# Optimization experiments

Hardware: AMD Instinct MI355X
Metric: run time of the kernel (lower is better)

## Reference

```python
import jax, jax.numpy as jnp
import numpy as np
from jax import lax

B, C_IN, C_OUT, L, K, PAD = 4, 16, 16, 1024, 5, 2


def setup_inputs() -> dict:
    key = jax.random.key(0)
    k1, k2 = jax.random.split(key)
    scores = jax.random.normal(k1, (B, C_IN, L, L), dtype=jnp.float32)
    # kaiming_uniform_(a=sqrt(5)) -> bound = 1/sqrt(fan_in), fan_in = (C_IN/groups)*K*K
    fan_in = C_IN * K * K
    bound = 1.0 / np.sqrt(fan_in)
    weight = jax.random.uniform(k2, (C_OUT, C_IN, K, K), dtype=jnp.float32,
                                minval=-bound, maxval=bound)
    bias = jnp.zeros((C_OUT,), dtype=jnp.float32)
    return {"scores": scores, "weight": weight, "bias": bias}


def reference(scores, weight, bias):
    # scores: [B, C_in, L, L]
    Lq = scores.shape[-2]
    causal = jnp.tril(jnp.ones((Lq, Lq), dtype=bool))  # [L, L]
    # mask_{-inf} then softmax over key dim
    masked = jnp.where(causal, scores, -jnp.inf)
    probs = jax.nn.softmax(masked, axis=-1)
    # grouped conv2d over the [L, L] score map (shape-preserving padding)
    out = lax.conv_general_dilated(
        probs, weight,
        window_strides=(1, 1),
        padding=((PAD, PAD), (PAD, PAD)),
        rhs_dilation=(1, 1),
        dimension_numbers=("NCHW", "OIHW", "NCHW"),
        feature_group_count=1,
    )
    out = out + bias[None, :, None, None]
    # mask_{0}: zero out non-causal positions
    out = jnp.where(causal, out, jnp.zeros((), dtype=out.dtype))
    return out
```

## Files before the change

kernel.cpp:

```cpp
#include <hip/hip_runtime.h>
#include <hip/hip_bf16.h>
#include <math.h>

#define LSEQ  1024
#define CIN   16
#define COUT  16
#define BATCH 4
#define TILE  16
#define NT    13
#define CSTR  48
#define RSTR  (20 * CSTR)

#define WFRAG_BYTES (NT * 64 * 8 * 2)
#define PROBS_ELEMS ((size_t)BATCH * CIN * LSEQ * LSEQ)
#define WS_NEEDED   (WFRAG_BYTES + PROBS_ELEMS * 2)

typedef __attribute__((ext_vector_type(8))) short short8;
typedef __attribute__((ext_vector_type(4))) float f32x4;
typedef __attribute__((ext_vector_type(4))) int   i32x4;

static __device__ __forceinline__ unsigned f2bf_u(float f) {
    unsigned u = __builtin_bit_cast(unsigned, f);
    return (u + 0x7fff + ((u >> 16) & 1)) >> 16;
}
static __device__ __forceinline__ unsigned short f2bf(float f) { return (unsigned short)f2bf_u(f); }

__global__ __launch_bounds__(256) void softmax_probs_kernel(
    const float* __restrict__ scores,
    const float* __restrict__ weight,
    ushort* __restrict__ wfrag,
    ushort* __restrict__ probs)
{
    const int tid = threadIdx.x;

    if (blockIdx.x == BATCH * LSEQ) {
        for (int slot = tid; slot < NT * 64; slot += 256) {
            const int t = slot >> 6, lane = slot & 63;
            const int co = lane & 15, q = lane >> 4;
            const int ci0 = (q & 1) * 8, cb = q >> 1;
            const int c = 2 * t + cb;
            ushort* dst = wfrag + (size_t)slot * 8;
            #pragma unroll
            for (int jj = 0; jj < 8; ++jj) {
                float wv = (c < 25) ? weight[co * (CIN * 25) + (ci0 + jj) * 25 + c] : 0.f;
                dst[jj] = f2bf(wv);
            }
        }
        return;
    }

    __shared__ ushort sm[CIN * LSEQ];

    const int bi   = blockIdx.x;
    const int b    = bi >> 10;
    const int row  = bi & (LSEQ - 1);
    const int wv   = tid >> 6;
    const int lane = tid & 63;

    #pragma unroll
    for (int m = 0; m < 4; ++m) {
        const int ci = wv * 4 + m;
        const float* rowp = scores + ((size_t)(b * CIN + ci) * LSEQ + row) * LSEQ;

        float e[16];
        #pragma unroll
        for (int c = 0; c < 4; ++c) {
            const int j0 = c * 256 + lane * 4;
            float4 v = make_float4(0.f, 0.f, 0.f, 0.f);
            if (c * 256 <= row) v = *(const float4*)(rowp + j0);
            e[c*4+0] = (j0 + 0 <= row) ? __expf(v.x) : 0.f;
            e[c*4+1] = (j0 + 1 <= row) ? __expf(v.y) : 0.f;
            e[c*4+2] = (j0 + 2 <= row) ? __expf(v.z) : 0.f;
            e[c*4+3] = (j0 + 3 <= row) ? __expf(v.w) : 0.f;
        }
        float s = 0.f;
        #pragma unroll
        for (int t = 0; t < 16; ++t) s += e[t];
        #pragma unroll
        for (int off = 32; off > 0; off >>= 1) s += __shfl_xor(s, off, 64);
        const float rinv = 1.0f / s;

        ushort* smrow = sm + ci * LSEQ;
        #pragma unroll
        for (int c = 0; c < 4; ++c) {
            if (c * 256 <= row) {
                const int j0 = c * 256 + lane * 4;
                uint2 pk;
                pk.x = f2bf_u(e[c*4+0] * rinv) | (f2bf_u(e[c*4+1] * rinv) << 16);
                pk.y = f2bf_u(e[c*4+2] * rinv) | (f2bf_u(e[c*4+3] * rinv) << 16);
                *(uint2*)(smrow + j0) = pk;
            }
        }
    }
    __syncthreads();

    ushort* prow = probs + ((size_t)b * LSEQ + row) * (LSEQ * CIN);
    const int nch = 2 * (row + 1);
    for (int chunk = tid; chunk < nch; chunk += 256) {
        const int col = chunk >> 1;
        const int h   = chunk & 1;
        i32x4 pk;
        #pragma unroll
        for (int k = 0; k < 4; ++k) {
            unsigned lo = sm[(h * 8 + 2 * k    ) * LSEQ + col];
            unsigned hi = sm[(h * 8 + 2 * k + 1) * LSEQ + col];
            pk[k] = (int)(lo | (hi << 16));
        }
        *(i32x4*)(prow + (size_t)col * CIN + h * 8) = pk;
    }
}

__global__ __launch_bounds__(256) void conv_mfma2_kernel(
    const ushort* __restrict__ probs,
    const float* __restrict__ bias,
    const ushort* __restrict__ wfrag,
    float* __restrict__ out)
{
    const int jt = blockIdx.x, it = blockIdx.y, b = blockIdx.z;
    const int j0 = jt * TILE, i0 = it * TILE;
    const int tid = threadIdx.x;

    if (jt > it) {
        #pragma unroll
        for (int vv = 0; vv < 4; ++vv) {
            int e  = vv * 256 + tid;
            int co = e >> 6, il = (e >> 2) & 15, jq = e & 3;
            *(float4*)(out + ((size_t)(b * COUT + co) * LSEQ + i0 + il) * LSEQ + j0 + jq * 4)
                = make_float4(0.f, 0.f, 0.f, 0.f);
        }
        return;
    }

    const int lane = tid & 63;
    const int w    = tid >> 6;
    const int n    = lane & 15;
    const int q    = lane >> 4;

    short8 af[NT];
    #pragma unroll
    for (int t = 0; t < NT; ++t)
        af[t] = *(const short8*)(wfrag + (size_t)(t * 64 + lane) * 8);

    float bs[4];
    #pragma unroll
    for (int r = 0; r < 4; ++r) bs[r] = bias[q * 4 + r];

    int addr[NT];
    {
        const int cb  = q >> 1;
        const int cio = (q & 1) * 16;
        #pragma unroll
        for (int t = 0; t < NT; ++t) {
            int c = 2 * t + cb;
            if (c >= 25) addr[t] = 0;
            else {
                int kh = c / 5, kw = c - kh * 5;
                addr[t] = (kh * 20 + (n + kw)) * CSTR + cio + w * (4 * RSTR);
            }
        }
    }

    __shared__ ushort ptile[20 * 20 * 24];

    const ushort* pb = probs + (size_t)b * (LSEQ * LSEQ * CIN);
    #pragma unroll
    for (int u = 0; u < 4; ++u) {
        const int e = u * 256 + tid;
        if (e < 800) {
            const int half = e & 1, cell = e >> 1;
            const int rr = cell / 20, cc = cell - rr * 20;
            const int row = i0 - 2 + rr;
            const int col = j0 - 2 + cc;
            const bool ok = (row >= 0) && (row < LSEQ) && (col >= 0) && (col < LSEQ) && (col <= row);
            i32x4 pk = {0, 0, 0, 0};
            if (ok)
                pk = *(const i32x4*)(pb + ((size_t)row * LSEQ + col) * CIN + half * 8);
            *(i32x4*)((char*)ptile + cell * CSTR + half * 16) = pk;
        }
    }
    __syncthreads();

    #pragma unroll
    for (int s = 0; s < 4; ++s) {
        f32x4 acc = {0.f, 0.f, 0.f, 0.f};
        #pragma unroll
        for (int t = 0; t < NT; ++t) {
            short8 bf = *(const short8*)((const char*)ptile + addr[t] + s * RSTR);
            acc = __builtin_amdgcn_mfma_f32_16x16x32_bf16(af[t], bf, acc, 0, 0, 0);
        }
        const int i = i0 + w * 4 + s;
        const int j = j0 + n;
        #pragma unroll
        for (int r = 0; r < 4; ++r) {
            const int co = q * 4 + r;
            out[((size_t)(b * COUT + co) * LSEQ + i) * LSEQ + j] = (j <= i) ? (acc[r] + bs[r]) : 0.f;
        }
    }
}

__global__ __launch_bounds__(256) void stats_fb_kernel(const float* __restrict__ scores,
                                                       float* __restrict__ rowinv)
{
    const int w   = blockIdx.x;
    const int row = w & (LSEQ - 1);
    const int tid = threadIdx.x;
    const int j0  = tid * 4;
    float4 v = make_float4(0.f, 0.f, 0.f, 0.f);
    if (j0 <= row) v = *(const float4*)(scores + (size_t)w * LSEQ + j0);
    float s = 0.f;
    s += (j0 + 0 <= row) ? __expf(v.x) : 0.f;
    s += (j0 + 1 <= row) ? __expf(v.y) : 0.f;
    s += (j0 + 2 <= row) ? __expf(v.z) : 0.f;
    s += (j0 + 3 <= row) ? __expf(v.w) : 0.f;
    #pragma unroll
    for (int off = 32; off > 0; off >>= 1) s += __shfl_xor(s, off, 64);
    __shared__ float part[4];
    if ((tid & 63) == 0) part[tid >> 6] = s;
    __syncthreads();
    if (tid == 0) rowinv[w] = 1.0f / (part[0] + part[1] + part[2] + part[3]);
}

__global__ void wprep_fb_kernel(const float* __restrict__ weight, ushort* __restrict__ wfrag)
{
    const int lane = threadIdx.x;
    const int co   = lane & 15;
    const int q    = lane >> 4;
    const int ci0  = (q & 1) * 8;
    const int cb   = q >> 1;
    for (int t = 0; t < NT; ++t) {
        const int c = 2 * t + cb;
        ushort* dst = wfrag + (size_t)(t * 64 + lane) * 8;
        #pragma unroll
        for (int jj = 0; jj < 8; ++jj) {
            float wv = (c < 25) ? weight[co * (CIN * 25) + (ci0 + jj) * 25 + c] : 0.f;
            dst[jj] = f2bf(wv);
        }
    }
}

__global__ __launch_bounds__(256) void conv_fb_kernel(
    const float* __restrict__ scores,
    const float* __restrict__ bias,
    const float* __restrict__ rowinv,
    const ushort* __restrict__ wfrag,
    float* __restrict__ out)
{
    const int jt = blockIdx.x, it = blockIdx.y, b = blockIdx.z;
    const int j0 = jt * TILE, i0 = it * TILE;
    const int tid = threadIdx.x;

    if (jt > it) {
        #pragma unroll
        for (int vv = 0; vv < 4; ++vv) {
            int e  = vv * 256 + tid;
            int co = e >> 6, il = (e >> 2) & 15, jq = e & 3;
            *(float4*)(out + ((size_t)(b * COUT + co) * LSEQ + i0 + il) * LSEQ + j0 + jq * 4)
                = make_float4(0.f, 0.f, 0.f, 0.f);
        }
        return;
    }

    const int lane = tid & 63;
    const int w    = tid >> 6;
    const int n    = lane & 15;
    const int q    = lane >> 4;

    short8 af[NT];
    #pragma unroll
    for (int t = 0; t < NT; ++t)
        af[t] = *(const short8*)(wfrag + (size_t)(t * 64 + lane) * 8);

    float bs[4];
    #pragma unroll
    for (int r = 0; r < 4; ++r) bs[r] = bias[q * 4 + r];

    int addr[NT];
    {
        const int cb  = q >> 1;
        const int cio = (q & 1) * 16;
        #pragma unroll
        for (int t = 0; t < NT; ++t) {
            int c = 2 * t + cb;
            if (c >= 25) addr[t] = 0;
            else {
                int kh = c / 5, kw = c - kh * 5;
                addr[t] = (kh * 20 + (n + kw)) * CSTR + cio + w * (4 * RSTR);
            }
        }
    }

    __shared__ ushort ptile[20 * 20 * 24];

    for (int u = 0; u < 8; ++u) {
        int e = u * 256 + tid;
        if (e < 1920) {
            int ci  = e / 120;
            int rem = e - ci * 120;
            int rr  = rem / 6;
            int cq  = rem - rr * 6;
            int row  = i0 - 2 + rr;
            int gcol = j0 - 4 + cq * 4;
            bool rok = (row >= 0) && (row < LSEQ);
            float rinv = 0.f;
            float4 v = make_float4(0.f, 0.f, 0.f, 0.f);
            if (rok) {
                int rid = (b * CIN + ci) * LSEQ + row;
                rinv = rowinv[rid];
                if (gcol >= 0 && gcol <= LSEQ - 4 && gcol <= row)
                    v = *(const float4*)(scores + (size_t)rid * LSEQ + gcol);
            }
            float pv[4] = {v.x, v.y, v.z, v.w};
            #pragma unroll
            for (int l = 0; l < 4; ++l) {
                int col = gcol + l;
                int cc  = cq * 4 - 2 + l;
                bool ok = rok && col >= 0 && col < LSEQ && col <= row;
                float p = ok ? __expf(pv[l]) * rinv : 0.f;
                if (cc >= 0 && cc < 20)
                    ptile[(rr * 20 + cc) * 24 + ci] = f2bf(p);
            }
        }
    }
    __syncthreads();

    #pragma unroll
    for (int s = 0; s < 4; ++s) {
        f32x4 acc = {0.f, 0.f, 0.f, 0.f};
        #pragma unroll
        for (int t = 0; t < NT; ++t) {
            short8 bf = *(const short8*)((const char*)ptile + addr[t] + s * RSTR);
            acc = __builtin_amdgcn_mfma_f32_16x16x32_bf16(af[t], bf, acc, 0, 0, 0);
        }
        const int i = i0 + w * 4 + s;
        const int j = j0 + n;
        #pragma unroll
        for (int r = 0; r < 4; ++r) {
            const int co = q * 4 + r;
            out[((size_t)(b * COUT + co) * LSEQ + i) * LSEQ + j] = (j <= i) ? (acc[r] + bs[r]) : 0.f;
        }
    }
}

extern "C" void kernel_launch(void* const* d_in, const int* in_sizes, int n_in,
                              void* d_out, int out_size, void* d_ws, size_t ws_size,
                              hipStream_t stream) {
    const float* scores = (const float*)d_in[0];
    const float* weight = (const float*)d_in[1];
    const float* bias   = (const float*)d_in[2];
    float* out = (float*)d_out;

    if (ws_size >= WS_NEEDED) {
        ushort* wfrag = (ushort*)d_ws;
        ushort* probs = (ushort*)((char*)d_ws + WFRAG_BYTES);

        softmax_probs_kernel<<<BATCH * LSEQ + 1, 256, 0, stream>>>(
            scores, weight, wfrag, probs);

        dim3 g(LSEQ / TILE, LSEQ / TILE, BATCH);
        conv_mfma2_kernel<<<g, 256, 0, stream>>>(probs, bias, wfrag, out);
    } else {
        float*  rowinv = (float*)d_ws;
        ushort* wfrag  = (ushort*)((char*)d_ws + (size_t)BATCH * CIN * LSEQ * 4);

        stats_fb_kernel<<<BATCH * CIN * LSEQ, 256, 0, stream>>>(scores, rowinv);
        wprep_fb_kernel<<<1, 64, 0, stream>>>(weight, wfrag);

        dim3 g(LSEQ / TILE, LSEQ / TILE, BATCH);
        conv_fb_kernel<<<g, 256, 0, stream>>>(scores, bias, rowinv, wfrag, out);
    }
}
```

Measured before the change: 521.2 us.

## Widen conv tile to 32 columns and swap MFMA operands for float4 stores

The conv kernel tile grows from 16x16 to 16 rows by 32 columns, so each block stages a 20x36 halo in LDS and reuses the loaded weight fragments across two 16-column subtiles. The MFMA operand order is swapped so each lane's accumulator holds four consecutive output columns for one channel, which allows vectorized float4 stores instead of scalar ones. This aims to reduce halo overhead, block count and store instructions, at the cost of more LDS per block and a coarser causal-skip granularity.

Result: no change. 530.6 us (+1.8%).

```diff
diff --git a/kernel.cpp b/kernel.cpp
--- a/kernel.cpp
+++ b/kernel.cpp
@@ -5,11 +5,14 @@
 #define LSEQ  1024
 #define CIN   16
 #define COUT  16
+#define TILE  16
+#define TJ    32
 #define BATCH 4
-#define TILE  16
 #define NT    13
 #define CSTR  48
+#define CW    36
 #define RSTR  (20 * CSTR)
+#define RSTR2 (CW * CSTR)
 
 #define WFRAG_BYTES (NT * 64 * 8 * 2)
 #define PROBS_ELEMS ((size_t)BATCH * CIN * LSEQ * LSEQ)
@@ -117,14 +120,14 @@
     float* __restrict__ out)
 {
     const int jt = blockIdx.x, it = blockIdx.y, b = blockIdx.z;
-    const int j0 = jt * TILE, i0 = it * TILE;
+    const int j0 = jt * TJ, i0 = it * TILE;
     const int tid = threadIdx.x;
 
-    if (jt > it) {
-        #pragma unroll
-        for (int vv = 0; vv < 4; ++vv) {
+    if (2 * jt > it) {
+        #pragma unroll
+        for (int vv = 0; vv < 8; ++vv) {
             int e  = vv * 256 + tid;
-            int co = e >> 6, il = (e >> 2) & 15, jq = e & 3;
+            int co = e >> 7, il = (e >> 3) & 15, jq = e & 7;
             *(float4*)(out + ((size_t)(b * COUT + co) * LSEQ + i0 + il) * LSEQ + j0 + jq * 4)
                 = make_float4(0.f, 0.f, 0.f, 0.f);
         }
@@ -141,9 +144,7 @@
     for (int t = 0; t < NT; ++t)
         af[t] = *(const short8*)(wfrag + (size_t)(t * 64 + lane) * 8);
 
-    float bs[4];
-    #pragma unroll
-    for (int r = 0; r < 4; ++r) bs[r] = bias[q * 4 + r];
+    const float bsn = bias[n];
 
     int addr[NT];
     {
@@ -155,20 +156,20 @@
             if (c >= 25) addr[t] = 0;
             else {
                 int kh = c / 5, kw = c - kh * 5;
-                addr[t] = (kh * 20 + (n + kw)) * CSTR + cio + w * (4 * RSTR);
-            }
-        }
-    }
-
-    __shared__ ushort ptile[20 * 20 * 24];
+                addr[t] = (kh * CW + (n + kw)) * CSTR + cio + w * (4 * RSTR2);
+            }
+        }
+    }
+
+    __shared__ ushort ptile[20 * CW * 24];
 
     const ushort* pb = probs + (size_t)b * (LSEQ * LSEQ * CIN);
     #pragma unroll
-    for (int u = 0; u < 4; ++u) {
+    for (int u = 0; u < 6; ++u) {
         const int e = u * 256 + tid;
-        if (e < 800) {
+        if (e < 1440) {
             const int half = e & 1, cell = e >> 1;
-            const int rr = cell / 20, cc = cell - rr * 20;
+            const int rr = cell / CW, cc = cell - rr * CW;
             const int row = i0 - 2 + rr;
             const int col = j0 - 2 + cc;
             const bool ok = (row >= 0) && (row < LSEQ) && (col >= 0) && (col < LSEQ) && (col <= row);
@@ -182,18 +183,22 @@
 
     #pragma unroll
     for (int s = 0; s < 4; ++s) {
-        f32x4 acc = {0.f, 0.f, 0.f, 0.f};
-        #pragma unroll
-        for (int t = 0; t < NT; ++t) {
-            short8 bf = *(const short8*)((const char*)ptile + addr[t] + s * RSTR);
-            acc = __builtin_amdgcn_mfma_f32_16x16x32_bf16(af[t], bf, acc, 0, 0, 0);
-        }
         const int i = i0 + w * 4 + s;
-        const int j = j0 + n;
-        #pragma unroll
-        for (int r = 0; r < 4; ++r) {
-            const int co = q * 4 + r;
-            out[((size_t)(b * COUT + co) * LSEQ + i) * LSEQ + j] = (j <= i) ? (acc[r] + bs[r]) : 0.f;
+        #pragma unroll
+        for (int sub = 0; sub < 2; ++sub) {
+            f32x4 acc = {0.f, 0.f, 0.f, 0.f};
+            #pragma unroll
+            for (int t = 0; t < NT; ++t) {
+                short8 pf = *(const short8*)((const char*)ptile + addr[t] + s * RSTR2 + sub * (16 * CSTR));
+                acc = __builtin_amdgcn_mfma_f32_16x16x32_bf16(pf, af[t], acc, 0, 0, 0);
+            }
+            const int jb = j0 + sub * 16 + q * 4;
+            float4 v;
+            v.x = (jb + 0 <= i) ? acc[0] + bsn : 0.f;
+            v.y = (jb + 1 <= i) ? acc[1] + bsn : 0.f;
+            v.z = (jb + 2 <= i) ? acc[2] + bsn : 0.f;
+            v.w = (jb + 3 <= i) ? acc[3] + bsn : 0.f;
+            *(float4*)(out + ((size_t)(b * COUT + n) * LSEQ + i) * LSEQ + jb) = v;
         }
     }
 }
@@ -356,7 +361,7 @@
         softmax_probs_kernel<<<BATCH * LSEQ + 1, 256, 0, stream>>>(
             scores, weight, wfrag, probs);
 
-        dim3 g(LSEQ / TILE, LSEQ / TILE, BATCH);
+        dim3 g(LSEQ / TJ, LSEQ / TILE, BATCH);
         conv_mfma2_kernel<<<g, 256, 0, stream>>>(probs, bias, wfrag, out);
     } else {
         float*  rowinv = (float*)d_ws;
```

## Load conv probability tile via global_load_lds and swap MFMA operands for vector stores

Applied to the files above, without the earlier changes.

The conv kernel now stages the 20x20 probability halo tile straight from global memory into LDS with global_load_lds, using a dense 32-byte cell stride. Out-of-range cells read from a zeroed pad placed after the weight fragments instead of being masked in registers. The MFMA operands are swapped so each lane holds four consecutive output columns for one channel, which lets the epilogue write float4 stores instead of scalar strided ones. The risks are that the removed LDS padding may bring back bank conflicts, and that the LDS destination layout must match what global_load_lds actually writes per wave.

After: 536.9 us. +3.0%, slower.

```diff
diff --git a/kernel.cpp b/kernel.cpp
--- a/kernel.cpp
+++ b/kernel.cpp
@@ -5,15 +5,18 @@
 #define LSEQ  1024
 #define CIN   16
 #define COUT  16
+#define TILE  16
 #define BATCH 4
-#define TILE  16
 #define NT    13
+#define CSTR2 32
+#define RSTR2 (20 * CSTR2)
 #define CSTR  48
 #define RSTR  (20 * CSTR)
 
 #define WFRAG_BYTES (NT * 64 * 8 * 2)
+#define ZPAD_BYTES  64
 #define PROBS_ELEMS ((size_t)BATCH * CIN * LSEQ * LSEQ)
-#define WS_NEEDED   (WFRAG_BYTES + PROBS_ELEMS * 2)
+#define WS_NEEDED   (WFRAG_BYTES + ZPAD_BYTES + PROBS_ELEMS * 2)
 
 typedef __attribute__((ext_vector_type(8))) short short8;
 typedef __attribute__((ext_vector_type(4))) float f32x4;
@@ -46,6 +49,7 @@
                 dst[jj] = f2bf(wv);
             }
         }
+        if (tid < 32) wfrag[NT * 64 * 8 + tid] = 0;
         return;
     }
 
@@ -141,9 +145,7 @@
     for (int t = 0; t < NT; ++t)
         af[t] = *(const short8*)(wfrag + (size_t)(t * 64 + lane) * 8);
 
-    float bs[4];
-    #pragma unroll
-    for (int r = 0; r < 4; ++r) bs[r] = bias[q * 4 + r];
+    const float bsn = bias[n];
 
     int addr[NT];
     {
@@ -155,28 +157,33 @@
             if (c >= 25) addr[t] = 0;
             else {
                 int kh = c / 5, kw = c - kh * 5;
-                addr[t] = (kh * 20 + (n + kw)) * CSTR + cio + w * (4 * RSTR);
-            }
-        }
-    }
-
-    __shared__ ushort ptile[20 * 20 * 24];
+                addr[t] = ((w * 4 + kh) * 20 + (n + kw)) * CSTR2 + cio;
+            }
+        }
+    }
+
+    __shared__ ushort ptile[1024 * 8];
 
     const ushort* pb = probs + (size_t)b * (LSEQ * LSEQ * CIN);
+    const ushort* zb = wfrag + NT * 64 * 8;
     #pragma unroll
     for (int u = 0; u < 4; ++u) {
         const int e = u * 256 + tid;
+        const ushort* src = zb;
         if (e < 800) {
-            const int half = e & 1, cell = e >> 1;
-            const int rr = cell / 20, cc = cell - rr * 20;
+            const int rr  = e / 40;
+            const int rem = e - rr * 40;
+            const int cc  = rem >> 1;
+            const int half = rem & 1;
             const int row = i0 - 2 + rr;
             const int col = j0 - 2 + cc;
             const bool ok = (row >= 0) && (row < LSEQ) && (col >= 0) && (col < LSEQ) && (col <= row);
-            i32x4 pk = {0, 0, 0, 0};
-            if (ok)
-                pk = *(const i32x4*)(pb + ((size_t)row * LSEQ + col) * CIN + half * 8);
-            *(i32x4*)((char*)ptile + cell * CSTR + half * 16) = pk;
-        }
+            if (ok) src = pb + ((size_t)row * LSEQ + col) * CIN + half * 8;
+        }
+        ushort* dst = ptile + (size_t)(u * 256 + (tid & 192)) * 8;
+        __builtin_amdgcn_global_load_lds(
+            (const __attribute__((address_space(1))) void*)src,
+            (__attribute__((address_space(3))) void*)dst, 16, 0, 0);
     }
     __syncthreads();
 
@@ -185,16 +192,17 @@
         f32x4 acc = {0.f, 0.f, 0.f, 0.f};
         #pragma unroll
         for (int t = 0; t < NT; ++t) {
-            short8 bf = *(const short8*)((const char*)ptile + addr[t] + s * RSTR);
-            acc = __builtin_amdgcn_mfma_f32_16x16x32_bf16(af[t], bf, acc, 0, 0, 0);
-        }
-        const int i = i0 + w * 4 + s;
-        const int j = j0 + n;
-        #pragma unroll
-        for (int r = 0; r < 4; ++r) {
-            const int co = q * 4 + r;
-            out[((size_t)(b * COUT + co) * LSEQ + i) * LSEQ + j] = (j <= i) ? (acc[r] + bs[r]) : 0.f;
-        }
+            short8 pf = *(const short8*)((const char*)ptile + addr[t] + s * RSTR2);
+            acc = __builtin_amdgcn_mfma_f32_16x16x32_bf16(pf, af[t], acc, 0, 0, 0);
+        }
+        const int i  = i0 + w * 4 + s;
+        const int jb = j0 + q * 4;
+        float4 v;
+        v.x = (jb + 0 <= i) ? acc[0] + bsn : 0.f;
+        v.y = (jb + 1 <= i) ? acc[1] + bsn : 0.f;
+        v.z = (jb + 2 <= i) ? acc[2] + bsn : 0.f;
+        v.w = (jb + 3 <= i) ? acc[3] + bsn : 0.f;
+        *(float4*)(out + ((size_t)(b * COUT + n) * LSEQ + i) * LSEQ + jb) = v;
     }
 }
 
@@ -351,7 +359,7 @@
 
     if (ws_size >= WS_NEEDED) {
         ushort* wfrag = (ushort*)d_ws;
-        ushort* probs = (ushort*)((char*)d_ws + WFRAG_BYTES);
+        ushort* probs = (ushort*)((char*)d_ws + WFRAG_BYTES + ZPAD_BYTES);
 
         softmax_probs_kernel<<<BATCH * LSEQ + 1, 256, 0, stream>>>(
             scores, weight, wfrag, probs);
```
